# Kernel optimization log

Measured on AMD Instinct MI355X. Metric: run time of the kernel, lower is better.

## Reference

```python
import jax, jax.numpy as jnp
import numpy as np

B, L, H, NH = 32, 512, 512, 8
HD = H // NH
SCALE = HD ** -0.5


def _heads(x):
    # (B, L, H) -> (B, NH, L, HD)
    return x.reshape(B, L, NH, HD).transpose(0, 2, 1, 3)


def _score(x, Wq, bq, Wk, bk):
    Q = _heads(x @ Wq.T + bq)
    K = _heads(x @ Wk.T + bk)
    return jnp.einsum('bhqd,bhkd->bhqk', Q, K) * SCALE


def setup_inputs() -> dict:
    key = jax.random.key(0)
    ks = jax.random.split(key, 16)
    d = {
        'seq_id': jax.random.normal(ks[0], (B, L, H), jnp.float32),
        'side_cate': jax.random.normal(ks[1], (B, L, H), jnp.float32),
        'side_brand': jax.random.normal(ks[2], (B, L, H), jnp.float32),
        'V_id_input': jax.random.normal(ks[3], (B, L, H), jnp.float32),
        'relative_time': jax.random.normal(ks[4], (B, NH, L, L), jnp.float32) * 0.02,
        'attn_mask': jnp.broadcast_to(jnp.tril(jnp.ones((L, L), bool)), (B, L, L)),
    }
    s = (2.0 / H) ** 0.5
    names = ['q_id', 'k_id', 'v', 'q_cate', 'k_cate', 'q_brand', 'k_brand', 'o']
    for i, n in enumerate(names):
        d['W' + n] = jax.random.normal(ks[5 + i], (H, H), jnp.float32) * s
        d['b' + n] = jnp.zeros((H,), jnp.float32)
    return d


def reference(seq_id, side_cate, side_brand, V_id_input, relative_time, attn_mask,
              Wq_id, bq_id, Wk_id, bk_id, Wv, bv,
              Wq_cate, bq_cate, Wk_cate, bk_cate,
              Wq_brand, bq_brand, Wk_brand, bk_brand,
              Wo, bo):
    V = _heads(V_id_input @ Wv.T + bv)  # (B, NH, L, HD)
    total = _score(seq_id, Wq_id, bq_id, Wk_id, bk_id)
    total = total + _score(side_cate, Wq_cate, bq_cate, Wk_cate, bk_cate)
    total = total + _score(side_brand, Wq_brand, bq_brand, Wk_brand, bk_brand)
    total = total + relative_time
    total = jnp.where(attn_mask[:, None], total, -jnp.inf)
    w = jax.nn.softmax(total.astype(jnp.float32), axis=-1).astype(total.dtype)
    w = jnp.nan_to_num(w, nan=0.0)
    # eval mode: dropout is identity
    attn_out = jnp.einsum('bhqk,bhkd->bhqd', w, V)
    attn_out = attn_out.transpose(0, 2, 1, 3).reshape(B, L, H)
    return attn_out @ Wo.T + bo
```

## Files before the change

kernel.cpp:

```cpp
#include <hip/hip_runtime.h>
#include <hip/hip_bf16.h>
#include <stdint.h>


typedef __bf16 bf16x8 __attribute__((ext_vector_type(8)));
typedef float f32x4 __attribute__((ext_vector_type(4)));

#define LOG2E 1.4426950408889634f

__device__ int g_isf32;

__device__ __forceinline__ f32x4 mfma16(bf16x8 a, bf16x8 b, f32x4 c) {
    return __builtin_amdgcn_mfma_f32_16x16x32_bf16(a, b, c, 0, 0, 0);
}

__device__ __forceinline__ float qmax16(float x) {
    x = fmaxf(x, __shfl_xor(x, 1));
    x = fmaxf(x, __shfl_xor(x, 2));
    x = fmaxf(x, __shfl_xor(x, 4));
    x = fmaxf(x, __shfl_xor(x, 8));
    return x;
}
__device__ __forceinline__ float qsum16(float x) {
    x += __shfl_xor(x, 1);
    x += __shfl_xor(x, 2);
    x += __shfl_xor(x, 4);
    x += __shfl_xor(x, 8);
    return x;
}

__device__ __forceinline__ bf16x8 ld8(const void* p, size_t off, int isf) {
    if (isf) {
        const float* f = (const float*)p + off;
        f32x4 a = *(const f32x4*)f;
        f32x4 b = *(const f32x4*)(f + 4);
        bf16x8 o;
        o[0] = (__bf16)a[0]; o[1] = (__bf16)a[1]; o[2] = (__bf16)a[2]; o[3] = (__bf16)a[3];
        o[4] = (__bf16)b[0]; o[5] = (__bf16)b[1]; o[6] = (__bf16)b[2]; o[7] = (__bf16)b[3];
        return o;
    }
    return *(const bf16x8*)((const __hip_bfloat16*)p + off);
}

__device__ __forceinline__ float ldf(const void* p, size_t off, int isf) {
    return isf ? ((const float*)p)[off]
               : __bfloat162float(((const __hip_bfloat16*)p)[off]);
}

__device__ __forceinline__ void glds16(const void* g, void* l) {
    __builtin_amdgcn_global_load_lds(
        (const __attribute__((address_space(1))) void*)g,
        (__attribute__((address_space(3))) void*)l, 16, 0, 0);
}

__global__ void sniff_kernel(const unsigned short* __restrict__ p) {
    int t = threadIdx.x;
    int bad = 0, zc = 0;
    #pragma unroll
    for (int i = 0; i < 32; i++) {
        unsigned short u = p[(t * 32 + i) * 2];
        int e = (u >> 7) & 0xFF;
        bad |= (e >= 0xF0);
        zc += (u == 0);
    }
    unsigned long long mb = __ballot(bad != 0);
    #pragma unroll
    for (int s = 1; s < 64; s <<= 1) zc += __shfl_xor(zc, s);
    if (t == 0) g_isf32 = (mb != 0ull || zc > 1024) ? 1 : 0;
}

__global__ __launch_bounds__(256) void conv3(
    const float* __restrict__ s0, const float* __restrict__ s1,
    const float* __restrict__ s2,
    __hip_bfloat16* __restrict__ d0, __hip_bfloat16* __restrict__ d1,
    __hip_bfloat16* __restrict__ d2)
{
    if (!g_isf32) return;
    const float* s = (blockIdx.z == 0) ? s0 : (blockIdx.z == 1) ? s1 : s2;
    __hip_bfloat16* d = (blockIdx.z == 0) ? d0 : (blockIdx.z == 1) ? d1 : d2;
    const int N8 = 32 * 512 * 512 / 8;
    for (int i = blockIdx.x * 256 + threadIdx.x; i < N8; i += gridDim.x * 256) {
        f32x4 a = ((const f32x4*)s)[2 * i];
        f32x4 b = ((const f32x4*)s)[2 * i + 1];
        bf16x8 o;
        o[0] = (__bf16)a[0]; o[1] = (__bf16)a[1]; o[2] = (__bf16)a[2]; o[3] = (__bf16)a[3];
        o[4] = (__bf16)b[0]; o[5] = (__bf16)b[1]; o[6] = (__bf16)b[2]; o[7] = (__bf16)b[3];
        ((bf16x8*)d)[i] = o;
    }
}

__global__ __launch_bounds__(256, 2) void gemm_all(
    const void* __restrict__ xs, const void* __restrict__ xc,
    const void* __restrict__ xb, const void* __restrict__ xv,
    const __hip_bfloat16* __restrict__ Xbs, const __hip_bfloat16* __restrict__ Xbc,
    const __hip_bfloat16* __restrict__ Xbb,
    const void* __restrict__ W0, const void* __restrict__ B0,
    const void* __restrict__ W1, const void* __restrict__ B1,
    const void* __restrict__ W2, const void* __restrict__ B2,
    const void* __restrict__ W3, const void* __restrict__ B3,
    const void* __restrict__ W4, const void* __restrict__ B4,
    const void* __restrict__ W5, const void* __restrict__ B5,
    const void* __restrict__ W6, const void* __restrict__ B6,
    const void* __restrict__ Wo, const void* __restrict__ Bo,
    const __hip_bfloat16* __restrict__ AO,
    __hip_bfloat16* __restrict__ Qcat, __hip_bfloat16* __restrict__ Kcat,
    __hip_bfloat16* __restrict__ Vt, void* __restrict__ Out,
    int oproj)
{
    __shared__ __align__(16) __hip_bfloat16 As[128 * 64];
    __shared__ __align__(16) __hip_bfloat16 Bs[128 * 64];

    const int isf = g_isf32;
    const int t = threadIdx.x;
    const int lane = t & 63, w = t >> 6;
    const int ln = lane & 15, hi = lane >> 4;
    const int wm = w >> 1, wn = w & 1;
    const int tm = blockIdx.x * 128, tn = blockIdx.y * 128;

    const __hip_bfloat16* Abf = nullptr;
    const void* Araw = nullptr;
    const void *W, *bias;
    int kind = 3, comp = 0;
    if (oproj) {
        Abf = AO; W = Wo; bias = Bo;
    } else {
        switch (blockIdx.z) {
            case 0:  Abf = isf ? Xbs : (const __hip_bfloat16*)xs;
                     W = W0; bias = B0; kind = 0; comp = 0; break;
            case 1:  Abf = isf ? Xbs : (const __hip_bfloat16*)xs;
                     W = W1; bias = B1; kind = 1; comp = 0; break;
            case 2:  if (isf) Araw = xv; else Abf = (const __hip_bfloat16*)xv;
                     W = W2; bias = B2; kind = 2; comp = 0; break;
            case 3:  Abf = isf ? Xbc : (const __hip_bfloat16*)xc;
                     W = W3; bias = B3; kind = 0; comp = 1; break;
            case 4:  Abf = isf ? Xbc : (const __hip_bfloat16*)xc;
                     W = W4; bias = B4; kind = 1; comp = 1; break;
            case 5:  Abf = isf ? Xbb : (const __hip_bfloat16*)xb;
                     W = W5; bias = B5; kind = 0; comp = 2; break;
            default: Abf = isf ? Xbb : (const __hip_bfloat16*)xb;
                     W = W6; bias = B6; kind = 1; comp = 2; break;
        }
    }

    f32x4 acc[4][4] = {};

    for (int k0 = 0; k0 < 512; k0 += 64) {
        #pragma unroll
        for (int r = 0; r < 4; r++) {
            int e = r * 2048 + t * 8;
            int row = e >> 6, col = e & 63;
            *(bf16x8*)&Bs[e] = ld8(W, (size_t)(tn + row) * 512 + k0 + col, isf);
        }
        if (Abf) {
            #pragma unroll
            for (int r = 0; r < 4; r++) {
                int e = r * 2048 + t * 8;
                int row = e >> 6, col = e & 63;
                glds16(Abf + (size_t)(tm + row) * 512 + k0 + col,
                       (char*)As + r * 4096 + w * 1024);
            }
        } else {
            #pragma unroll
            for (int r = 0; r < 4; r++) {
                int e = r * 2048 + t * 8;
                int row = e >> 6, col = e & 63;
                *(bf16x8*)&As[e] = ld8(Araw, (size_t)(tm + row) * 512 + k0 + col, 1);
            }
        }
        __syncthreads();

        #pragma unroll
        for (int kk = 0; kk < 64; kk += 32) {
            bf16x8 af[4], bfr[4];
            #pragma unroll
            for (int i = 0; i < 4; i++)
                af[i] = *(const bf16x8*)&As[(wm * 64 + i * 16 + ln) * 64 + kk + hi * 8];
            #pragma unroll
            for (int j = 0; j < 4; j++)
                bfr[j] = *(const bf16x8*)&Bs[(wn * 64 + j * 16 + ln) * 64 + kk + hi * 8];
            #pragma unroll
            for (int i = 0; i < 4; i++)
                #pragma unroll
                for (int j = 0; j < 4; j++)
                    acc[i][j] = mfma16(af[i], bfr[j], acc[i][j]);
        }
        __syncthreads();
    }

    #pragma unroll
    for (int j = 0; j < 4; j++) {
        int col = tn + wn * 64 + j * 16 + ln;
        float bv = ldf(bias, col, isf);
        int h = col >> 6, d = col & 63;
        #pragma unroll
        for (int i = 0; i < 4; i++) {
            #pragma unroll
            for (int r = 0; r < 4; r++) {
                int row = tm + wm * 64 + i * 16 + hi * 4 + r;
                float val = acc[i][j][r] + bv;
                int b = row >> 9, l = row & 511;
                if (kind == 0)
                    Qcat[((size_t)(b * 8 + h) * 512 + l) * 192 + comp * 64 + d] =
                        __float2bfloat16(val);
                else if (kind == 1)
                    Kcat[((size_t)(b * 8 + h) * 512 + l) * 192 + comp * 64 + d] =
                        __float2bfloat16(val);
                else if (kind == 2)
                    Vt[((size_t)(b * 8 + h) * 64 + d) * 512 + l] =
                        __float2bfloat16(val);
                else if (isf)
                    ((float*)Out)[(size_t)row * 512 + col] = val;
                else
                    ((__hip_bfloat16*)Out)[(size_t)row * 512 + col] =
                        __float2bfloat16(val);
            }
        }
    }
}

__global__ __launch_bounds__(256, 2) void attn_kernel(
    const __hip_bfloat16* __restrict__ Qcat,
    const __hip_bfloat16* __restrict__ Kcat,
    const __hip_bfloat16* __restrict__ Vt,
    const void* __restrict__ rel,
    __hip_bfloat16* __restrict__ AO)
{
    __shared__ __align__(16) __hip_bfloat16 Ks[64 * 208];
    __shared__ __align__(16) __hip_bfloat16 Vs[64 * 80];
    __shared__ __align__(16) __hip_bfloat16 Ps[4 * 32 * 80];

    const int isf = g_isf32;
    const int t = threadIdx.x;
    const int lane = t & 63, w = t >> 6;
    const int ln = lane & 15, hi = lane >> 4;
    const int qt = blockIdx.x, h = blockIdx.y, b = blockIdx.z;
    const int qb = qt * 128;
    const size_t bh = (size_t)(b * 8 + h);

    const __hip_bfloat16* qc = Qcat + bh * 512 * 192;
    const __hip_bfloat16* kc = Kcat + bh * 512 * 192;
    const __hip_bfloat16* vp = Vt + bh * 64 * 512;
    const size_t rbase = bh * 512 * 512;

    bf16x8 qf[2][6];
    #pragma unroll
    for (int i = 0; i < 2; i++)
        #pragma unroll
        for (int kf = 0; kf < 6; kf++)
            qf[i][kf] = *(const bf16x8*)(qc + (size_t)(qb + w * 32 + i * 16 + ln) * 192
                                            + kf * 32 + hi * 8);

    float mst[2][4], lst[2][4];
    f32x4 oacc[2][4] = {};
    #pragma unroll
    for (int i = 0; i < 2; i++)
        #pragma unroll
        for (int r = 0; r < 4; r++) { mst[i][r] = -1e30f; lst[i][r] = 0.f; }

    const int nkt = 2 * qt + 2;
    for (int kt = 0; kt < nkt; kt++) {
        const int kb = kt * 64;
        __syncthreads();

        #pragma unroll
        for (int r = 0; r < 6; r++) {
            int e = r * 2048 + t * 8;
            int row = e / 192, col = e - row * 192;
            bf16x8 v = *(const bf16x8*)(kc + (size_t)(kb + row) * 192 + col);
            *(bf16x8*)&Ks[row * 208 + col] = v;
        }
        #pragma unroll
        for (int r = 0; r < 2; r++) {
            int e = r * 2048 + t * 8;
            int row = e >> 6, col = e & 63;
            bf16x8 v = *(const bf16x8*)(vp + (size_t)row * 512 + kb + col);
            *(bf16x8*)&Vs[row * 80 + col] = v;
        }
        __syncthreads();

        f32x4 s[2][4] = {};
        #pragma unroll
        for (int kf = 0; kf < 6; kf++) {
            bf16x8 bfr[4];
            #pragma unroll
            for (int j = 0; j < 4; j++)
                bfr[j] = *(const bf16x8*)&Ks[(j * 16 + ln) * 208 + kf * 32 + hi * 8];
            #pragma unroll
            for (int i = 0; i < 2; i++)
                #pragma unroll
                for (int j = 0; j < 4; j++)
                    s[i][j] = mfma16(qf[i][kf], bfr[j], s[i][j]);
        }

        #pragma unroll
        for (int i = 0; i < 2; i++) {
            #pragma unroll
            for (int r = 0; r < 4; r++) {
                int qrow = qb + w * 32 + i * 16 + hi * 4 + r;
                size_t roff = rbase + (size_t)qrow * 512 + kb;
                #pragma unroll
                for (int j = 0; j < 4; j++) {
                    int col = kb + j * 16 + ln;
                    float rv = ldf(rel, roff + j * 16 + ln, isf);
                    float v = fmaf(s[i][j][r], 0.125f * LOG2E, rv * LOG2E);
                    s[i][j][r] = (col > qrow) ? -1e30f : v;
                }
            }
        }

        #pragma unroll
        for (int i = 0; i < 2; i++) {
            #pragma unroll
            for (int r = 0; r < 4; r++) {
                float mx = fmaxf(fmaxf(s[i][0][r], s[i][1][r]),
                                 fmaxf(s[i][2][r], s[i][3][r]));
                mx = qmax16(mx);
                float mnew = fmaxf(mst[i][r], mx);
                float al = exp2f(mst[i][r] - mnew);
                float sum = 0.f;
                #pragma unroll
                for (int j = 0; j < 4; j++) {
                    float p = exp2f(s[i][j][r] - mnew);
                    s[i][j][r] = p;
                    sum += p;
                }
                sum = qsum16(sum);
                lst[i][r] = lst[i][r] * al + sum;
                mst[i][r] = mnew;
                #pragma unroll
                for (int jn = 0; jn < 4; jn++)
                    oacc[i][jn][r] *= al;
            }
        }

        __hip_bfloat16* pw = &Ps[w * 32 * 80];
        #pragma unroll
        for (int i = 0; i < 2; i++) {
            #pragma unroll
            for (int r = 0; r < 4; r++) {
                int prow = i * 16 + hi * 4 + r;
                #pragma unroll
                for (int j = 0; j < 4; j++)
                    pw[prow * 80 + j * 16 + ln] = __float2bfloat16(s[i][j][r]);
            }
        }
        __syncthreads();

        #pragma unroll
        for (int kk = 0; kk < 64; kk += 32) {
            bf16x8 ap[2], bv[4];
            #pragma unroll
            for (int i = 0; i < 2; i++)
                ap[i] = *(const bf16x8*)&Ps[w * 2560 + (i * 16 + ln) * 80 + kk + hi * 8];
            #pragma unroll
            for (int jn = 0; jn < 4; jn++)
                bv[jn] = *(const bf16x8*)&Vs[(jn * 16 + ln) * 80 + kk + hi * 8];
            #pragma unroll
            for (int i = 0; i < 2; i++)
                #pragma unroll
                for (int jn = 0; jn < 4; jn++)
                    oacc[i][jn] = mfma16(ap[i], bv[jn], oacc[i][jn]);
        }
    }

    #pragma unroll
    for (int i = 0; i < 2; i++) {
        #pragma unroll
        for (int r = 0; r < 4; r++) {
            int qrow = qb + w * 32 + i * 16 + hi * 4 + r;
            float inv = 1.0f / lst[i][r];
            __hip_bfloat16* orow = AO + ((size_t)(b * 512 + qrow)) * 512 + h * 64;
            #pragma unroll
            for (int jn = 0; jn < 4; jn++)
                orow[jn * 16 + ln] = __float2bfloat16(oacc[i][jn][r] * inv);
        }
    }
}

extern "C" void kernel_launch(void* const* d_in, const int* in_sizes, int n_in,
                              void* d_out, int out_size, void* d_ws, size_t ws_size,
                              hipStream_t stream) {
    (void)in_sizes; (void)n_in; (void)out_size; (void)ws_size;
    const void* xs  = d_in[0];
    const void* xc  = d_in[1];
    const void* xb  = d_in[2];
    const void* xv  = d_in[3];
    const void* rel = d_in[4];
    const void* W0 = d_in[6];    const void* B0 = d_in[7];
    const void* W1 = d_in[8];    const void* B1 = d_in[9];
    const void* W2 = d_in[10];   const void* B2 = d_in[11];
    const void* W3 = d_in[12];   const void* B3 = d_in[13];
    const void* W4 = d_in[14];   const void* B4 = d_in[15];
    const void* W5 = d_in[16];   const void* B5 = d_in[17];
    const void* W6 = d_in[18];   const void* B6 = d_in[19];
    const void* Wo = d_in[20];   const void* Bo = d_in[21];

    char* ws = (char*)d_ws;
    __hip_bfloat16* Qcat = (__hip_bfloat16*)(ws);
    __hip_bfloat16* Kcat = (__hip_bfloat16*)(ws + 50331648);
    __hip_bfloat16* Vt   = (__hip_bfloat16*)(ws + 100663296);
    __hip_bfloat16* AO   = (__hip_bfloat16*)(ws + 117440512);

    __hip_bfloat16* Xbs = AO;
    __hip_bfloat16* Xbc = (__hip_bfloat16*)d_out;
    __hip_bfloat16* Xbb = (__hip_bfloat16*)((char*)d_out + 16777216);

    dim3 blk(256, 1, 1);
    sniff_kernel<<<1, 64, 0, stream>>>((const unsigned short*)xs);
    conv3<<<dim3(1024, 1, 3), blk, 0, stream>>>(
        (const float*)xs, (const float*)xc, (const float*)xb, Xbs, Xbc, Xbb);
    gemm_all<<<dim3(128, 4, 7), blk, 0, stream>>>(
        xs, xc, xb, xv, Xbs, Xbc, Xbb,
        W0, B0, W1, B1, W2, B2, W3, B3, W4, B4, W5, B5, W6, B6,
        Wo, Bo, AO, Qcat, Kcat, Vt, d_out, 0);
    attn_kernel<<<dim3(4, 8, 32), blk, 0, stream>>>(Qcat, Kcat, Vt, rel, AO);
    gemm_all<<<dim3(128, 4, 1), blk, 0, stream>>>(
        xs, xc, xb, xv, Xbs, Xbc, Xbb,
        W0, B0, W1, B1, W2, B2, W3, B3, W4, B4, W5, B5, W6, B6,
        Wo, Bo, AO, Qcat, Kcat, Vt, d_out, 1);
}
```

Measured before the change: 775.5 us.

## Pre-convert weights to bf16, double-buffer GEMM with swizzled async LDS loads

The change adds a kernel that converts all eight fp32 weight matrices to bf16 once, and extends the input conversion to cover V. With every operand now in bf16, the GEMM can load both A and B straight into LDS with global_load_lds, using double buffering, an XOR-swizzled column layout and explicit vmcnt waits, so the next tile's loads overlap the MFMAs. The attention kernel gets tighter LDS padding and s_setprio around its MFMA sections. The cost is two extra conversion passes and extra global buffers, and the hand-written waitcnt and barrier sequence is fragile.

```diff
diff --git a/kernel.cpp b/kernel.cpp
--- a/kernel.cpp
+++ b/kernel.cpp
@@ -9,6 +9,8 @@
 #define LOG2E 1.4426950408889634f
 
 __device__ int g_isf32;
+__device__ __align__(16) unsigned short g_Wbf[8 * 512 * 512];
+__device__ __align__(16) unsigned short g_Xbv[32 * 512 * 512];
 
 __device__ __forceinline__ f32x4 mfma16(bf16x8 a, bf16x8 b, f32x4 c) {
     return __builtin_amdgcn_mfma_f32_16x16x32_bf16(a, b, c, 0, 0, 0);
@@ -29,19 +31,6 @@
     return x;
 }
 
-__device__ __forceinline__ bf16x8 ld8(const void* p, size_t off, int isf) {
-    if (isf) {
-        const float* f = (const float*)p + off;
-        f32x4 a = *(const f32x4*)f;
-        f32x4 b = *(const f32x4*)(f + 4);
-        bf16x8 o;
-        o[0] = (__bf16)a[0]; o[1] = (__bf16)a[1]; o[2] = (__bf16)a[2]; o[3] = (__bf16)a[3];
-        o[4] = (__bf16)b[0]; o[5] = (__bf16)b[1]; o[6] = (__bf16)b[2]; o[7] = (__bf16)b[3];
-        return o;
-    }
-    return *(const bf16x8*)((const __hip_bfloat16*)p + off);
-}
-
 __device__ __forceinline__ float ldf(const void* p, size_t off, int isf) {
     return isf ? ((const float*)p)[off]
                : __bfloat162float(((const __hip_bfloat16*)p)[off]);
@@ -69,15 +58,17 @@
     if (t == 0) g_isf32 = (mb != 0ull || zc > 1024) ? 1 : 0;
 }
 
-__global__ __launch_bounds__(256) void conv3(
+__global__ __launch_bounds__(256) void conv4(
     const float* __restrict__ s0, const float* __restrict__ s1,
-    const float* __restrict__ s2,
+    const float* __restrict__ s2, const float* __restrict__ s3,
     __hip_bfloat16* __restrict__ d0, __hip_bfloat16* __restrict__ d1,
     __hip_bfloat16* __restrict__ d2)
 {
     if (!g_isf32) return;
-    const float* s = (blockIdx.z == 0) ? s0 : (blockIdx.z == 1) ? s1 : s2;
-    __hip_bfloat16* d = (blockIdx.z == 0) ? d0 : (blockIdx.z == 1) ? d1 : d2;
+    const int z = blockIdx.z;
+    const float* s = (z == 0) ? s0 : (z == 1) ? s1 : (z == 2) ? s2 : s3;
+    __hip_bfloat16* d = (z == 0) ? d0 : (z == 1) ? d1 : (z == 2) ? d2
+                                      : (__hip_bfloat16*)g_Xbv;
     const int N8 = 32 * 512 * 512 / 8;
     for (int i = blockIdx.x * 256 + threadIdx.x; i < N8; i += gridDim.x * 256) {
         f32x4 a = ((const f32x4*)s)[2 * i];
@@ -87,6 +78,30 @@
         o[4] = (__bf16)b[0]; o[5] = (__bf16)b[1]; o[6] = (__bf16)b[2]; o[7] = (__bf16)b[3];
         ((bf16x8*)d)[i] = o;
     }
+}
+
+__global__ __launch_bounds__(256) void convW(
+    const float* __restrict__ W0, const float* __restrict__ W1,
+    const float* __restrict__ W2, const float* __restrict__ W3,
+    const float* __restrict__ W4, const float* __restrict__ W5,
+    const float* __restrict__ W6, const float* __restrict__ Wo)
+{
+    if (!g_isf32) return;
+    const int z = blockIdx.z;
+    const float* src;
+    switch (z) {
+        case 0: src = W0; break; case 1: src = W1; break;
+        case 2: src = W2; break; case 3: src = W3; break;
+        case 4: src = W4; break; case 5: src = W5; break;
+        case 6: src = W6; break; default: src = Wo; break;
+    }
+    int i = blockIdx.x * 256 + threadIdx.x;
+    f32x4 a = ((const f32x4*)src)[2 * i];
+    f32x4 b = ((const f32x4*)src)[2 * i + 1];
+    bf16x8 o;
+    o[0] = (__bf16)a[0]; o[1] = (__bf16)a[1]; o[2] = (__bf16)a[2]; o[3] = (__bf16)a[3];
+    o[4] = (__bf16)b[0]; o[5] = (__bf16)b[1]; o[6] = (__bf16)b[2]; o[7] = (__bf16)b[3];
+    ((bf16x8*)g_Wbf)[z * 32768 + i] = o;
 }
 
 __global__ __launch_bounds__(256, 2) void gemm_all(
@@ -107,8 +122,8 @@
     __hip_bfloat16* __restrict__ Vt, void* __restrict__ Out,
     int oproj)
 {
-    __shared__ __align__(16) __hip_bfloat16 As[128 * 64];
-    __shared__ __align__(16) __hip_bfloat16 Bs[128 * 64];
+    __shared__ __align__(16) __hip_bfloat16 As[2][128 * 64];
+    __shared__ __align__(16) __hip_bfloat16 Bs[2][128 * 64];
 
     const int isf = g_isf32;
     const int t = threadIdx.x;
@@ -117,75 +132,87 @@
     const int wm = w >> 1, wn = w & 1;
     const int tm = blockIdx.x * 128, tn = blockIdx.y * 128;
 
-    const __hip_bfloat16* Abf = nullptr;
-    const void* Araw = nullptr;
+    const __hip_bfloat16* Ab;
     const void *W, *bias;
-    int kind = 3, comp = 0;
+    int kind = 3, comp = 0, wslot = 7;
     if (oproj) {
-        Abf = AO; W = Wo; bias = Bo;
+        Ab = AO; W = Wo; bias = Bo;
     } else {
         switch (blockIdx.z) {
-            case 0:  Abf = isf ? Xbs : (const __hip_bfloat16*)xs;
-                     W = W0; bias = B0; kind = 0; comp = 0; break;
-            case 1:  Abf = isf ? Xbs : (const __hip_bfloat16*)xs;
-                     W = W1; bias = B1; kind = 1; comp = 0; break;
-            case 2:  if (isf) Araw = xv; else Abf = (const __hip_bfloat16*)xv;
-                     W = W2; bias = B2; kind = 2; comp = 0; break;
-            case 3:  Abf = isf ? Xbc : (const __hip_bfloat16*)xc;
-                     W = W3; bias = B3; kind = 0; comp = 1; break;
-            case 4:  Abf = isf ? Xbc : (const __hip_bfloat16*)xc;
-                     W = W4; bias = B4; kind = 1; comp = 1; break;
-            case 5:  Abf = isf ? Xbb : (const __hip_bfloat16*)xb;
-                     W = W5; bias = B5; kind = 0; comp = 2; break;
-            default: Abf = isf ? Xbb : (const __hip_bfloat16*)xb;
-                     W = W6; bias = B6; kind = 1; comp = 2; break;
-        }
-    }
+            case 0:  Ab = isf ? Xbs : (const __hip_bfloat16*)xs;
+                     W = W0; bias = B0; kind = 0; comp = 0; wslot = 0; break;
+            case 1:  Ab = isf ? Xbs : (const __hip_bfloat16*)xs;
+                     W = W1; bias = B1; kind = 1; comp = 0; wslot = 1; break;
+            case 2:  Ab = isf ? (const __hip_bfloat16*)g_Xbv : (const __hip_bfloat16*)xv;
+                     W = W2; bias = B2; kind = 2; comp = 0; wslot = 2; break;
+            case 3:  Ab = isf ? Xbc : (const __hip_bfloat16*)xc;
+                     W = W3; bias = B3; kind = 0; comp = 1; wslot = 3; break;
+            case 4:  Ab = isf ? Xbc : (const __hip_bfloat16*)xc;
+                     W = W4; bias = B4; kind = 1; comp = 1; wslot = 4; break;
+            case 5:  Ab = isf ? Xbb : (const __hip_bfloat16*)xb;
+                     W = W5; bias = B5; kind = 0; comp = 2; wslot = 5; break;
+            default: Ab = isf ? Xbb : (const __hip_bfloat16*)xb;
+                     W = W6; bias = B6; kind = 1; comp = 2; wslot = 6; break;
+        }
+    }
+    const __hip_bfloat16* Wb = isf ? (const __hip_bfloat16*)g_Wbf + (size_t)wslot * 262144
+                                   : (const __hip_bfloat16*)W;
+
+    const int csw = (((lane & 7) ^ ((lane >> 3) & 7)) * 8);
+    const int rsub = (w * 8) + (lane >> 3);
 
     f32x4 acc[4][4] = {};
 
-    for (int k0 = 0; k0 < 512; k0 += 64) {
-        #pragma unroll
-        for (int r = 0; r < 4; r++) {
-            int e = r * 2048 + t * 8;
-            int row = e >> 6, col = e & 63;
-            *(bf16x8*)&Bs[e] = ld8(W, (size_t)(tn + row) * 512 + k0 + col, isf);
-        }
-        if (Abf) {
-            #pragma unroll
-            for (int r = 0; r < 4; r++) {
-                int e = r * 2048 + t * 8;
-                int row = e >> 6, col = e & 63;
-                glds16(Abf + (size_t)(tm + row) * 512 + k0 + col,
-                       (char*)As + r * 4096 + w * 1024);
-            }
-        } else {
-            #pragma unroll
-            for (int r = 0; r < 4; r++) {
-                int e = r * 2048 + t * 8;
-                int row = e >> 6, col = e & 63;
-                *(bf16x8*)&As[e] = ld8(Araw, (size_t)(tm + row) * 512 + k0 + col, 1);
-            }
-        }
-        __syncthreads();
-
+    #define STAGE(bi, kt)                                                        \
+        do {                                                                     \
+            int _k0 = (kt) * 64;                                                 \
+            _Pragma("unroll")                                                    \
+            for (int r = 0; r < 4; r++)                                          \
+                glds16(Ab + (size_t)(tm + r * 32 + rsub) * 512 + _k0 + csw,      \
+                       (char*)&As[bi][0] + r * 4096 + w * 1024);                 \
+            _Pragma("unroll")                                                    \
+            for (int r = 0; r < 4; r++)                                          \
+                glds16(Wb + (size_t)(tn + r * 32 + rsub) * 512 + _k0 + csw,      \
+                       (char*)&Bs[bi][0] + r * 4096 + w * 1024);                 \
+        } while (0)
+
+    STAGE(0, 0);
+    STAGE(1, 1);
+    asm volatile("s_waitcnt vmcnt(8)" ::: "memory");
+    __builtin_amdgcn_s_barrier();
+
+    for (int k = 0; k < 8; k++) {
+        const int cur = k & 1;
+        asm volatile("" ::: "memory");
+        const __hip_bfloat16* Asc = &As[cur][0];
+        const __hip_bfloat16* Bsc = &Bs[cur][0];
         #pragma unroll
         for (int kk = 0; kk < 64; kk += 32) {
             bf16x8 af[4], bfr[4];
             #pragma unroll
             for (int i = 0; i < 4; i++)
-                af[i] = *(const bf16x8*)&As[(wm * 64 + i * 16 + ln) * 64 + kk + hi * 8];
+                af[i] = *(const bf16x8*)&Asc[(wm * 64 + i * 16 + ln) * 64 +
+                                             ((kk + hi * 8) ^ ((ln & 7) * 8))];
             #pragma unroll
             for (int j = 0; j < 4; j++)
-                bfr[j] = *(const bf16x8*)&Bs[(wn * 64 + j * 16 + ln) * 64 + kk + hi * 8];
+                bfr[j] = *(const bf16x8*)&Bsc[(wn * 64 + j * 16 + ln) * 64 +
+                                              ((kk + hi * 8) ^ ((ln & 7) * 8))];
             #pragma unroll
             for (int i = 0; i < 4; i++)
                 #pragma unroll
                 for (int j = 0; j < 4; j++)
                     acc[i][j] = mfma16(af[i], bfr[j], acc[i][j]);
         }
-        __syncthreads();
-    }
+        __builtin_amdgcn_s_barrier();
+        if (k + 2 < 8) {
+            STAGE(cur, k + 2);
+            asm volatile("s_waitcnt vmcnt(8)" ::: "memory");
+        } else {
+            asm volatile("s_waitcnt vmcnt(0)" ::: "memory");
+        }
+        __builtin_amdgcn_s_barrier();
+    }
+    #undef STAGE
 
     #pragma unroll
     for (int j = 0; j < 4; j++) {
@@ -225,9 +252,9 @@
     const void* __restrict__ rel,
     __hip_bfloat16* __restrict__ AO)
 {
-    __shared__ __align__(16) __hip_bfloat16 Ks[64 * 208];
-    __shared__ __align__(16) __hip_bfloat16 Vs[64 * 80];
-    __shared__ __align__(16) __hip_bfloat16 Ps[4 * 32 * 80];
+    __shared__ __align__(16) __hip_bfloat16 Ks[64 * 200];
+    __shared__ __align__(16) __hip_bfloat16 Vs[64 * 72];
+    __shared__ __align__(16) __hip_bfloat16 Ps[4 * 32 * 72];
 
     const int isf = g_isf32;
     const int t = threadIdx.x;
@@ -267,30 +294,32 @@
             int e = r * 2048 + t * 8;
             int row = e / 192, col = e - row * 192;
             bf16x8 v = *(const bf16x8*)(kc + (size_t)(kb + row) * 192 + col);
-            *(bf16x8*)&Ks[row * 208 + col] = v;
+            *(bf16x8*)&Ks[row * 200 + col] = v;
         }
         #pragma unroll
         for (int r = 0; r < 2; r++) {
             int e = r * 2048 + t * 8;
             int row = e >> 6, col = e & 63;
             bf16x8 v = *(const bf16x8*)(vp + (size_t)row * 512 + kb + col);
-            *(bf16x8*)&Vs[row * 80 + col] = v;
+            *(bf16x8*)&Vs[row * 72 + col] = v;
         }
         __syncthreads();
 
         f32x4 s[2][4] = {};
+        __builtin_amdgcn_s_setprio(1);
         #pragma unroll
         for (int kf = 0; kf < 6; kf++) {
             bf16x8 bfr[4];
             #pragma unroll
             for (int j = 0; j < 4; j++)
-                bfr[j] = *(const bf16x8*)&Ks[(j * 16 + ln) * 208 + kf * 32 + hi * 8];
+                bfr[j] = *(const bf16x8*)&Ks[(j * 16 + ln) * 200 + kf * 32 + hi * 8];
             #pragma unroll
             for (int i = 0; i < 2; i++)
                 #pragma unroll
                 for (int j = 0; j < 4; j++)
                     s[i][j] = mfma16(qf[i][kf], bfr[j], s[i][j]);
         }
+        __builtin_amdgcn_s_setprio(0);
 
         #pragma unroll
         for (int i = 0; i < 2; i++) {
@@ -333,7 +362,7 @@
             }
         }
 
-        __hip_bfloat16* pw = &Ps[w * 32 * 80];
+        __hip_bfloat16* pw = &Ps[w * 32 * 72];
         #pragma unroll
         for (int i = 0; i < 2; i++) {
             #pragma unroll
@@ -341,26 +370,28 @@
                 int prow = i * 16 + hi * 4 + r;
                 #pragma unroll
                 for (int j = 0; j < 4; j++)
-                    pw[prow * 80 + j * 16 + ln] = __float2bfloat16(s[i][j][r]);
+                    pw[prow * 72 + j * 16 + ln] = __float2bfloat16(s[i][j][r]);
             }
         }
         __syncthreads();
 
+        __builtin_amdgcn_s_setprio(1);
         #pragma unroll
         for (int kk = 0; kk < 64; kk += 32) {
             bf16x8 ap[2], bv[4];
             #pragma unroll
             for (int i = 0; i < 2; i++)
-                ap[i] = *(const bf16x8*)&Ps[w * 2560 + (i * 16 + ln) * 80 + kk + hi * 8];
+                ap[i] = *(const bf16x8*)&Ps[w * 2304 + (i * 16 + ln) * 72 + kk + hi * 8];
             #pragma unroll
             for (int jn = 0; jn < 4; jn++)
-                bv[jn] = *(const bf16x8*)&Vs[(jn * 16 + ln) * 80 + kk + hi * 8];
+                bv[jn] = *(const bf16x8*)&Vs[(jn * 16 + ln) * 72 + kk + hi * 8];
             #pragma unroll
             for (int i = 0; i < 2; i++)
                 #pragma unroll
                 for (int jn = 0; jn < 4; jn++)
                     oacc[i][jn] = mfma16(ap[i], bv[jn], oacc[i][jn]);
         }
+        __builtin_amdgcn_s_setprio(0);
     }
 
     #pragma unroll
@@ -407,8 +438,12 @@
 
     dim3 blk(256, 1, 1);
     sniff_kernel<<<1, 64, 0, stream>>>((const unsigned short*)xs);
-    conv3<<<dim3(1024, 1, 3), blk, 0, stream>>>(
-        (const float*)xs, (const float*)xc, (const float*)xb, Xbs, Xbc, Xbb);
+    conv4<<<dim3(1024, 1, 4), blk, 0, stream>>>(
+        (const float*)xs, (const float*)xc, (const float*)xb, (const float*)xv,
+        Xbs, Xbc, Xbb);
+    convW<<<dim3(128, 1, 8), blk, 0, stream>>>(
+        (const float*)W0, (const float*)W1, (const float*)W2, (const float*)W3,
+        (const float*)W4, (const float*)W5, (const float*)W6, (const float*)Wo);
     gemm_all<<<dim3(128, 4, 7), blk, 0, stream>>>(
         xs, xc, xb, xv, Xbs, Xbc, Xbb,
         W0, B0, W1, B1, W2, B2, W3, B3, W4, B4, W5, B5, W6, B6,
```

New measurement: 682.0 us. -12.1%, faster.
